# Performance work log

Hardware: AMD Instinct MI355X
Metric: run time of the kernel (lower is better)

## Reference

```python
import jax, jax.numpy as jnp
import numpy as np

N_ATOMS = 64
NC2 = N_ATOMS * (N_ATOMS - 1) // 2  # 2016
BATCH = 32768


def setup_inputs() -> dict:
    key = jax.random.key(0)
    decompFE = jax.random.normal(key, (BATCH, NC2), dtype=jnp.float32)
    return {"decompFE": decompFE}


def reference(decompFE):
    # Flat NC2 values map to strict lower triangle positions in row-major
    # order: (1,0),(2,0),(2,1),(3,0),... which is exactly jnp.tril_indices(n,-1).
    b, nc2 = decompFE.shape
    n = N_ATOMS
    rows, cols = jnp.tril_indices(n, k=-1)  # each length NC2, row-major order
    # Scatter flat values into strict lower triangle of [b, n, n]
    lower = jnp.zeros((b, n, n), dtype=decompFE.dtype).at[:, rows, cols].set(decompFE)
    # Symmetrize (diagonal stays zero)
    return lower + jnp.swapaxes(lower, -1, -2)
```

## Files before the change

### kernel.cpp

```cpp
#include <hip/hip_runtime.h>

constexpr int N_ATOMS = 64;
constexpr int NC2 = N_ATOMS * (N_ATOMS - 1) / 2;
constexpr int BATCH = 32768;

__global__ __launch_bounds__(256) void triangle_kernel(
    const float* __restrict__ in, float* __restrict__ out) {
    __shared__ float sm[NC2];

    const int b = blockIdx.x;
    const int t = threadIdx.x;

    const float4* in4 = reinterpret_cast<const float4*>(in + (size_t)b * NC2);
    float4* sm4 = reinterpret_cast<float4*>(sm);
#pragma unroll
    for (int it = 0; it < 2; ++it) {
        int idx = it * 256 + t;
        if (idx < NC2 / 4) {
            sm4[idx] = in4[idx];
        }
    }
    __syncthreads();

    float4* out4 = reinterpret_cast<float4*>(out + (size_t)b * N_ATOMS * N_ATOMS);
#pragma unroll
    for (int it = 0; it < 4; ++it) {
        int e4 = it * 256 + t;
        int e = e4 * 4;
        int i = e >> 6;
        int j0 = e & 63;

        int base_lower = i * (i - 1) / 2;

        float vv[4];
#pragma unroll
        for (int k = 0; k < 4; ++k) {
            int j = j0 + k;
            float val;
            if (j < i) {
                val = sm[base_lower + j];
            } else if (j > i) {
                val = sm[j * (j - 1) / 2 + i];
            } else {
                val = 0.0f;
            }
            vv[k] = val;
        }
        out4[e4] = make_float4(vv[0], vv[1], vv[2], vv[3]);
    }
}

extern "C" void kernel_launch(void* const* d_in, const int* in_sizes, int n_in,
                              void* d_out, int out_size, void* d_ws, size_t ws_size,
                              hipStream_t stream) {
    const float* in = (const float*)d_in[0];
    float* out = (float*)d_out;
    triangle_kernel<<<BATCH, 256, 0, stream>>>(in, out);
}
```

Baseline: 673.2 us.

## Scatter triangle into swizzled full shared matrix and emit vectorized nontemporal stores

Each thread now scatters its loaded input values into both (i,j) and (j,i) slots of a full 64x64 shared-memory matrix. A rotated column swizzle is meant to avoid bank conflicts on those writes. The output phase then becomes one vectorized LDS read and one nontemporal global store per float4, with no per-element branching or index arithmetic. In exchange, row and column indices are derived from a float sqrt with integer correction, and shared-memory writes double.

New measurement: 690.6 us. 1.03x slower.

```diff
diff --git a/kernel.cpp b/kernel.cpp
--- a/kernel.cpp
+++ b/kernel.cpp
@@ -1,4 +1,6 @@
 #include <hip/hip_runtime.h>
+
+typedef float v4f __attribute__((ext_vector_type(4)));
 
 constexpr int N_ATOMS = 64;
 constexpr int NC2 = N_ATOMS * (N_ATOMS - 1) / 2;
@@ -6,47 +8,48 @@
 
 __global__ __launch_bounds__(256) void triangle_kernel(
     const float* __restrict__ in, float* __restrict__ out) {
-    __shared__ float sm[NC2];
+    __shared__ float sm[N_ATOMS * 64];
 
     const int b = blockIdx.x;
     const int t = threadIdx.x;
 
-    const float4* in4 = reinterpret_cast<const float4*>(in + (size_t)b * NC2);
-    float4* sm4 = reinterpret_cast<float4*>(sm);
+    if (t < N_ATOMS) {
+        sm[t * 64 + ((5 * t) & 63)] = 0.0f;
+    }
+
+    const v4f* in4 = reinterpret_cast<const v4f*>(in + (size_t)b * NC2);
 #pragma unroll
     for (int it = 0; it < 2; ++it) {
         int idx = it * 256 + t;
         if (idx < NC2 / 4) {
-            sm4[idx] = in4[idx];
+            v4f v = in4[idx];
+            int p = idx * 4;
+            int i = (int)((1.0f + sqrtf(8.0f * (float)p + 1.0f)) * 0.5f);
+            if (i * (i - 1) / 2 > p) --i;
+            if ((i + 1) * i / 2 <= p) ++i;
+            int j = p - i * (i - 1) / 2;
+#pragma unroll
+            for (int k = 0; k < 4; ++k) {
+                float val = v[k];
+                sm[i * 64 + ((j + 4 * i) & 63)] = val;
+                sm[j * 64 + ((i + 4 * j) & 63)] = val;
+                ++j;
+                if (j == i) { ++i; j = 0; }
+            }
         }
     }
     __syncthreads();
 
-    float4* out4 = reinterpret_cast<float4*>(out + (size_t)b * N_ATOMS * N_ATOMS);
+    float* outp = out + (size_t)b * N_ATOMS * N_ATOMS;
+    const v4f* sm4 = reinterpret_cast<const v4f*>(sm);
+    v4f* out4 = reinterpret_cast<v4f*>(outp);
 #pragma unroll
     for (int it = 0; it < 4; ++it) {
-        int e4 = it * 256 + t;
-        int e = e4 * 4;
-        int i = e >> 6;
-        int j0 = e & 63;
-
-        int base_lower = i * (i - 1) / 2;
-
-        float vv[4];
-#pragma unroll
-        for (int k = 0; k < 4; ++k) {
-            int j = j0 + k;
-            float val;
-            if (j < i) {
-                val = sm[base_lower + j];
-            } else if (j > i) {
-                val = sm[j * (j - 1) / 2 + i];
-            } else {
-                val = 0.0f;
-            }
-            vv[k] = val;
-        }
-        out4[e4] = make_float4(vv[0], vv[1], vv[2], vv[3]);
+        int q = it * 256 + t;
+        int i = q >> 4;
+        int jq = q & 15;
+        v4f v = sm4[i * 16 + ((jq + i) & 15)];
+        __builtin_nontemporal_store(v, out4 + q);
     }
 }
 
```
